# Optimization experiments

Hardware: AMD Instinct MI355X
Metric: run time of the kernel (lower is better)

The kernel has to match this reference:

```python
import jax, jax.numpy as jnp
import numpy as np

TEMPERATURE = 0.5


def setup_inputs() -> dict:
    key = jax.random.key(0)
    k1, k2 = jax.random.split(key)
    N, D = 4096, 512
    emb_i = jax.random.normal(k1, (N, D), dtype=jnp.float32)
    emb_j = jax.random.normal(k2, (N, D), dtype=jnp.float32)
    return {"emb_i": emb_i, "emb_j": emb_j}


def reference(emb_i, emb_j):
    # L2-normalize each embedding row (F.normalize, dim=1)
    z_i = emb_i / jnp.linalg.norm(emb_i, axis=1, keepdims=True)
    z_j = emb_j / jnp.linalg.norm(emb_j, axis=1, keepdims=True)
    reps = jnp.concatenate([z_i, z_j], axis=0)  # [2N, D]
    N = emb_i.shape[0]
    M = 2 * N
    # cosine similarity of normalized vectors == dot product -> [2N, 2N]
    sim = jnp.einsum('id,jd->ij', reps, reps) / TEMPERATURE
    # denominator: sum_k!=i exp(sim[i,k]); original multiplies by one-hot complement
    exp_sim = jnp.exp(sim)
    denom = jnp.sum(exp_sim, axis=1) - jnp.diagonal(exp_sim)  # [2N]
    log_denom = jnp.log(denom)
    # positive pairs: (k, k+N) and (k+N, k)
    idx = jnp.arange(N)
    pos_ij = sim[idx, idx + N]          # sim(k, k+N)/T
    pos_ji = sim[idx + N, idx]          # sim(k+N, k)/T
    loss = jnp.sum(-(pos_ij - log_denom[:N]) - (pos_ji - log_denom[N:]))
    return loss / (2.0 * N)
```

## Files before the change

### kernel.cpp

```cpp
#include <hip/hip_runtime.h>
#include <cstdint>
#include <cstddef>

constexpr int N_ROWS = 4096;
constexpr int D      = 512;
constexpr int M      = 8192;
constexpr int NTILE  = 64;
constexpr int NBLK   = NTILE * (NTILE + 1) / 2;

using f32x4  = __attribute__((ext_vector_type(4))) float;
using bf16x8 = __attribute__((ext_vector_type(8))) __bf16;
using us8    = __attribute__((ext_vector_type(8))) unsigned short;

__device__ inline unsigned short f2bf(float f) {
    unsigned int u = __float_as_uint(f);
    u += 0x7fffu + ((u >> 16) & 1u);
    return (unsigned short)(u >> 16);
}
__device__ inline float bf2f(unsigned short s) {
    return __uint_as_float(((unsigned int)s) << 16);
}

#define ASYNC_CP16(gsrc, ldst)                                                      \
    __builtin_amdgcn_global_load_lds(                                               \
        (const __attribute__((address_space(1))) unsigned int*)(gsrc),              \
        (__attribute__((address_space(3))) unsigned int*)(ldst), 16, 0, 0)

__global__ __launch_bounds__(256) void normpos_kernel(
    const float* __restrict__ emb_i, const float* __restrict__ emb_j,
    unsigned short* __restrict__ zb, float* __restrict__ diagss,
    float* __restrict__ pos)
{
    const int wave = threadIdx.x >> 6, lane = threadIdx.x & 63;
    const int k = blockIdx.x * 4 + wave;

    const float4* a = (const float4*)(emb_i + (size_t)k * D);
    const float4* b = (const float4*)(emb_j + (size_t)k * D);
    float4 a0 = a[lane * 2], a1 = a[lane * 2 + 1];
    float4 b0 = b[lane * 2], b1 = b[lane * 2 + 1];

    float ssi = a0.x*a0.x + a0.y*a0.y + a0.z*a0.z + a0.w*a0.w
              + a1.x*a1.x + a1.y*a1.y + a1.z*a1.z + a1.w*a1.w;
    float ssj = b0.x*b0.x + b0.y*b0.y + b0.z*b0.z + b0.w*b0.w
              + b1.x*b1.x + b1.y*b1.y + b1.z*b1.z + b1.w*b1.w;
    float dp  = a0.x*b0.x + a0.y*b0.y + a0.z*b0.z + a0.w*b0.w
              + a1.x*b1.x + a1.y*b1.y + a1.z*b1.z + a1.w*b1.w;
    #pragma unroll
    for (int off = 32; off; off >>= 1) {
        ssi += __shfl_xor(ssi, off, 64);
        ssj += __shfl_xor(ssj, off, 64);
        dp  += __shfl_xor(dp,  off, 64);
    }
    const float invi = rsqrtf(ssi), invj = rsqrtf(ssj);

    const float zi[8] = {a0.x*invi, a0.y*invi, a0.z*invi, a0.w*invi,
                         a1.x*invi, a1.y*invi, a1.z*invi, a1.w*invi};
    const float zj[8] = {b0.x*invj, b0.y*invj, b0.z*invj, b0.w*invj,
                         b1.x*invj, b1.y*invj, b1.z*invj, b1.w*invj};
    us8 pi, pj;
    float dssi = 0.f, dssj = 0.f;
    #pragma unroll
    for (int t = 0; t < 8; ++t) {
        unsigned short bi = f2bf(zi[t]), bj = f2bf(zj[t]);
        pi[t] = bi; pj[t] = bj;
        float fi = bf2f(bi), fj = bf2f(bj);
        dssi += fi * fi; dssj += fj * fj;
    }
    *(us8*)(zb + (size_t)k * D + lane * 8)            = pi;
    *(us8*)(zb + (size_t)(k + N_ROWS) * D + lane * 8) = pj;
    #pragma unroll
    for (int off = 32; off; off >>= 1) {
        dssi += __shfl_xor(dssi, off, 64);
        dssj += __shfl_xor(dssj, off, 64);
    }
    if (lane == 0) {
        diagss[k]          = dssi;
        diagss[k + N_ROWS] = dssj;
        pos[k]             = 2.0f * dp * invi * invj;
    }
}

__global__ __launch_bounds__(256, 4) void simgemm_kernel(
    const unsigned short* __restrict__ zb, float* __restrict__ partials)
{
    __shared__ unsigned short As[128 * 32];
    __shared__ unsigned short Bs[128 * 32];
    __shared__ float rp[4][64];
    __shared__ float cp4[4][64];
    const int tid  = threadIdx.x;
    const int wave = tid >> 6, lane = tid & 63;
    const int l15  = lane & 15, ks = lane >> 4;

    const int t = blockIdx.x;
    int bi = (int)((129.0f - sqrtf(129.0f * 129.0f - 8.0f * (float)t)) * 0.5f);
    while (bi > 0 && bi * (129 - bi) / 2 > t) --bi;
    while ((bi + 1) * (129 - (bi + 1)) / 2 <= t) ++bi;
    const int bj = bi + (t - bi * (129 - bi) / 2);
    const bool diag = (bi == bj);

    const int wrow = (wave >> 1) * 64, wcol = (wave & 1) * 64;

    const int ch0 = wave * 2;
    const int sr0 = ch0 * 16 + (lane >> 2);
    const int sc  = ((lane & 3) ^ ((sr0 >> 1) & 3)) * 8;
    const unsigned short* gA0 = zb + (size_t)(bi * 128 + sr0) * D + sc;
    const unsigned short* gB0 = zb + (size_t)(bj * 128 + sr0) * D + sc;
    unsigned short* lA0 = As + ch0 * 512;
    unsigned short* lA1 = As + ch0 * 512 + 512;
    unsigned short* lB0 = Bs + ch0 * 512;
    unsigned short* lB1 = Bs + ch0 * 512 + 512;

    f32x4 acc[4][4] = {};
    const int swOff = (ks ^ ((l15 >> 1) & 3)) * 8;

    for (int kc = 0; kc < D; kc += 32) {
        ASYNC_CP16(gA0 + kc,          lA0);
        ASYNC_CP16(gA0 + kc + 16 * D, lA1);
        ASYNC_CP16(gB0 + kc,          lB0);
        ASYNC_CP16(gB0 + kc + 16 * D, lB1);
        __syncthreads();

        bf16x8 af[4], bg[4];
        #pragma unroll
        for (int f = 0; f < 4; ++f) {
            af[f] = *(const bf16x8*)(As + (wrow + f * 16 + l15) * 32 + swOff);
            bg[f] = *(const bf16x8*)(Bs + (wcol + f * 16 + l15) * 32 + swOff);
        }
        #pragma unroll
        for (int i = 0; i < 4; ++i)
            #pragma unroll
            for (int j = 0; j < 4; ++j)
                acc[i][j] = __builtin_amdgcn_mfma_f32_16x16x32_bf16(
                    af[i], bg[j], acc[i][j], 0, 0, 0);
        __syncthreads();
    }

    float rowp[4][4] = {};
    #pragma unroll
    for (int j = 0; j < 4; ++j) {
        float cpj = 0.f;
        #pragma unroll
        for (int i = 0; i < 4; ++i)
            #pragma unroll
            for (int r = 0; r < 4; ++r) {
                float e = __expf(2.0f * acc[i][j][r]);
                rowp[i][r] += e;
                cpj += e;
            }
        if (!diag) {
            cpj += __shfl_xor(cpj, 16, 64);
            cpj += __shfl_xor(cpj, 32, 64);
            if (ks == 0) cp4[wave][j * 16 + l15] = cpj;
        }
    }
    #pragma unroll
    for (int i = 0; i < 4; ++i)
        #pragma unroll
        for (int r = 0; r < 4; ++r) {
            float e = rowp[i][r];
            e += __shfl_xor(e, 1, 64);
            e += __shfl_xor(e, 2, 64);
            e += __shfl_xor(e, 4, 64);
            e += __shfl_xor(e, 8, 64);
            if (l15 == 0) rp[wave][i * 16 + ks * 4 + r] = e;
        }
    __syncthreads();

    float* pA = partials + (size_t)(bi * NTILE + bj) * 128;
    float* pB = partials + (size_t)(bj * NTILE + bi) * 128;
    if (tid < 128) {
        const int h = tid >> 6, rr = tid & 63;
        pA[tid] = rp[h * 2][rr] + rp[h * 2 + 1][rr];
    } else if (!diag) {
        const int c = tid - 128, h = c >> 6, cc = c & 63;
        pB[c] = cp4[h][cc] + cp4[h + 2][cc];
    }
}

__global__ __launch_bounds__(256) void rowfin_kernel(
    const float* __restrict__ partials, const float* __restrict__ diagss,
    float* __restrict__ lgpart)
{
    const int r  = blockIdx.x;
    const int ri = threadIdx.x & 127;
    const int ch = threadIdx.x >> 7;
    const float* base = partials + (size_t)r * NTILE * 128 + ri;
    float s = 0.f;
    #pragma unroll
    for (int c = 0; c < 32; ++c)
        s += base[(size_t)(ch * 32 + c) * 128];
    __shared__ float half1[128];
    __shared__ float red[4];
    if (ch == 1) half1[ri] = s;
    __syncthreads();
    float lg = 0.f;
    if (ch == 0) {
        float rs = s + half1[ri];
        int row = r * 128 + ri;
        lg = __logf(rs - __expf(2.0f * diagss[row]));
    }
    #pragma unroll
    for (int off = 32; off; off >>= 1) lg += __shfl_xor(lg, off, 64);
    const int wave = threadIdx.x >> 6, lane = threadIdx.x & 63;
    if (lane == 0) red[wave] = lg;
    __syncthreads();
    if (threadIdx.x == 0) lgpart[r] = red[0] + red[1] + red[2] + red[3];
}

__global__ __launch_bounds__(256) void loss_kernel(
    const float* __restrict__ lgpart, const float* __restrict__ pos,
    float* __restrict__ out)
{
    float local = 0.f;
    if (threadIdx.x < NTILE) local += lgpart[threadIdx.x];
    for (int k = threadIdx.x; k < N_ROWS; k += 256)
        local -= 2.0f * pos[k];
    #pragma unroll
    for (int off = 32; off; off >>= 1) local += __shfl_xor(local, off, 64);
    __shared__ float red[4];
    const int wave = threadIdx.x >> 6, lane = threadIdx.x & 63;
    if (lane == 0) red[wave] = local;
    __syncthreads();
    if (threadIdx.x == 0)
        out[0] = (red[0] + red[1] + red[2] + red[3]) * (1.0f / 8192.0f);
}

extern "C" void kernel_launch(void* const* d_in, const int* in_sizes, int n_in,
                              void* d_out, int out_size, void* d_ws, size_t ws_size,
                              hipStream_t stream)
{
    const float* emb_i = (const float*)d_in[0];
    const float* emb_j = (const float*)d_in[1];

    unsigned short* zb = (unsigned short*)d_ws;
    float* partials = (float*)((char*)d_ws + (size_t)M * D * sizeof(unsigned short));
    float* diagss   = partials + (size_t)NTILE * NTILE * 128;
    float* pos      = diagss + M;
    float* lgpart   = pos + N_ROWS;
    float* out      = (float*)d_out;

    normpos_kernel<<<N_ROWS / 4, 256, 0, stream>>>(emb_i, emb_j, zb, diagss, pos);
    simgemm_kernel<<<NBLK, 256, 0, stream>>>(zb, partials);
    rowfin_kernel<<<NTILE, 256, 0, stream>>>(partials, diagss, lgpart);
    loss_kernel<<<1, 256, 0, stream>>>(lgpart, pos, out);
}
```

Before: 126.0 us.

## Double-buffer LDS tiles in sim GEMM and fold positive-pair sum into rowfin

The similarity GEMM now keeps two LDS buffers, prefetching the next K-chunk with async global-to-LDS copies while MFMAs consume the current one. This drops one barrier per iteration and hides load latency. The positive-pair subtraction moves from the single-block loss kernel into rowfin, so the final kernel becomes a one-wave reduction. The risks are the doubled LDS footprint, which may limit occupancy at 4 blocks per CU, and the correctness of async-copy completion ordering relative to the single barrier.

```diff
diff --git a/kernel.cpp b/kernel.cpp
--- a/kernel.cpp
+++ b/kernel.cpp
@@ -7,6 +7,7 @@
 constexpr int M      = 8192;
 constexpr int NTILE  = 64;
 constexpr int NBLK   = NTILE * (NTILE + 1) / 2;
+constexpr int LDSOFF = 128 * 32;
 
 using f32x4  = __attribute__((ext_vector_type(4))) float;
 using bf16x8 = __attribute__((ext_vector_type(8))) __bf16;
@@ -83,8 +84,8 @@
 __global__ __launch_bounds__(256, 4) void simgemm_kernel(
     const unsigned short* __restrict__ zb, float* __restrict__ partials)
 {
-    __shared__ unsigned short As[128 * 32];
-    __shared__ unsigned short Bs[128 * 32];
+    __shared__ unsigned short As[2 * 128 * 32];
+    __shared__ unsigned short Bs[2 * 128 * 32];
     __shared__ float rp[4][64];
     __shared__ float cp4[4][64];
     const int tid  = threadIdx.x;
@@ -105,26 +106,36 @@
     const int sc  = ((lane & 3) ^ ((sr0 >> 1) & 3)) * 8;
     const unsigned short* gA0 = zb + (size_t)(bi * 128 + sr0) * D + sc;
     const unsigned short* gB0 = zb + (size_t)(bj * 128 + sr0) * D + sc;
-    unsigned short* lA0 = As + ch0 * 512;
-    unsigned short* lA1 = As + ch0 * 512 + 512;
-    unsigned short* lB0 = Bs + ch0 * 512;
-    unsigned short* lB1 = Bs + ch0 * 512 + 512;
+    unsigned short* lA = As + ch0 * 512;
+    unsigned short* lB = Bs + ch0 * 512;
+
+    ASYNC_CP16(gA0,          lA);
+    ASYNC_CP16(gA0 + 16 * D, lA + 512);
+    ASYNC_CP16(gB0,          lB);
+    ASYNC_CP16(gB0 + 16 * D, lB + 512);
 
     f32x4 acc[4][4] = {};
     const int swOff = (ks ^ ((l15 >> 1) & 3)) * 8;
 
-    for (int kc = 0; kc < D; kc += 32) {
-        ASYNC_CP16(gA0 + kc,          lA0);
-        ASYNC_CP16(gA0 + kc + 16 * D, lA1);
-        ASYNC_CP16(gB0 + kc,          lB0);
-        ASYNC_CP16(gB0 + kc + 16 * D, lB1);
+    #pragma unroll 2
+    for (int it = 0; it < D / 32; ++it) {
         __syncthreads();
 
+        if (it + 1 < D / 32) {
+            const int kc  = (it + 1) * 32;
+            const int off = ((it + 1) & 1) * LDSOFF;
+            ASYNC_CP16(gA0 + kc,          lA + off);
+            ASYNC_CP16(gA0 + kc + 16 * D, lA + off + 512);
+            ASYNC_CP16(gB0 + kc,          lB + off);
+            ASYNC_CP16(gB0 + kc + 16 * D, lB + off + 512);
+        }
+
+        const int cb = (it & 1) * LDSOFF;
         bf16x8 af[4], bg[4];
         #pragma unroll
         for (int f = 0; f < 4; ++f) {
-            af[f] = *(const bf16x8*)(As + (wrow + f * 16 + l15) * 32 + swOff);
-            bg[f] = *(const bf16x8*)(Bs + (wcol + f * 16 + l15) * 32 + swOff);
+            af[f] = *(const bf16x8*)(As + cb + (wrow + f * 16 + l15) * 32 + swOff);
+            bg[f] = *(const bf16x8*)(Bs + cb + (wcol + f * 16 + l15) * 32 + swOff);
         }
         #pragma unroll
         for (int i = 0; i < 4; ++i)
@@ -132,7 +143,6 @@
             for (int j = 0; j < 4; ++j)
                 acc[i][j] = __builtin_amdgcn_mfma_f32_16x16x32_bf16(
                     af[i], bg[j], acc[i][j], 0, 0, 0);
-        __syncthreads();
     }
 
     float rowp[4][4] = {};
@@ -179,7 +189,7 @@
 
 __global__ __launch_bounds__(256) void rowfin_kernel(
     const float* __restrict__ partials, const float* __restrict__ diagss,
-    float* __restrict__ lgpart)
+    const float* __restrict__ pos, float* __restrict__ lgpart)
 {
     const int r  = blockIdx.x;
     const int ri = threadIdx.x & 127;
@@ -199,6 +209,8 @@
         int row = r * 128 + ri;
         lg = __logf(rs - __expf(2.0f * diagss[row]));
     }
+    if (threadIdx.x < 64)
+        lg -= 2.0f * pos[r * 64 + threadIdx.x];
     #pragma unroll
     for (int off = 32; off; off >>= 1) lg += __shfl_xor(lg, off, 64);
     const int wave = threadIdx.x >> 6, lane = threadIdx.x & 63;
@@ -207,22 +219,13 @@
     if (threadIdx.x == 0) lgpart[r] = red[0] + red[1] + red[2] + red[3];
 }
 
-__global__ __launch_bounds__(256) void loss_kernel(
-    const float* __restrict__ lgpart, const float* __restrict__ pos,
-    float* __restrict__ out)
-{
-    float local = 0.f;
-    if (threadIdx.x < NTILE) local += lgpart[threadIdx.x];
-    for (int k = threadIdx.x; k < N_ROWS; k += 256)
-        local -= 2.0f * pos[k];
+__global__ __launch_bounds__(64) void loss_kernel(
+    const float* __restrict__ lgpart, float* __restrict__ out)
+{
+    float local = lgpart[threadIdx.x];
     #pragma unroll
     for (int off = 32; off; off >>= 1) local += __shfl_xor(local, off, 64);
-    __shared__ float red[4];
-    const int wave = threadIdx.x >> 6, lane = threadIdx.x & 63;
-    if (lane == 0) red[wave] = local;
-    __syncthreads();
-    if (threadIdx.x == 0)
-        out[0] = (red[0] + red[1] + red[2] + red[3]) * (1.0f / 8192.0f);
+    if (threadIdx.x == 0) out[0] = local * (1.0f / 8192.0f);
 }
 
 extern "C" void kernel_launch(void* const* d_in, const int* in_sizes, int n_in,
@@ -241,6 +244,6 @@
 
     normpos_kernel<<<N_ROWS / 4, 256, 0, stream>>>(emb_i, emb_j, zb, diagss, pos);
     simgemm_kernel<<<NBLK, 256, 0, stream>>>(zb, partials);
-    rowfin_kernel<<<NTILE, 256, 0, stream>>>(partials, diagss, lgpart);
-    loss_kernel<<<1, 256, 0, stream>>>(lgpart, pos, out);
-}
+    rowfin_kernel<<<NTILE, 256, 0, stream>>>(partials, diagss, pos, lgpart);
+    loss_kernel<<<1, 64, 0, stream>>>(lgpart, out);
+}
```

After: 122.4 us. -2.9%, faster.
